# Optimization experiments

Measured on AMD Instinct MI355X. Metric: run time of the kernel, lower is better.

The kernel has to match this reference:

```python
import jax, jax.numpy as jnp
import numpy as np

B, T, C = 2, 2048, 1024
N_HEAD = 16
HEAD_DIM = C // N_HEAD


def setup_inputs() -> dict:
    key = jax.random.key(0)
    k1, k2, k3 = jax.random.split(key, 3)
    s = 1.0 / np.sqrt(C)
    return {
        "x": jax.random.normal(k1, (B, T, C), dtype=jnp.float32),
        "w_qkv": jax.random.normal(k2, (C, 3 * C), dtype=jnp.float32) * s,
        "b_qkv": jnp.zeros((3 * C,), dtype=jnp.float32),
        "w_out": jax.random.normal(k3, (C, C), dtype=jnp.float32) * s,
        "b_out": jnp.zeros((C,), dtype=jnp.float32),
    }


def reference(x, w_qkv, b_qkv, w_out, b_out):
    b, t, c = x.shape
    qkv = x @ w_qkv + b_qkv                                   # [B,T,3C]
    # Faithful to torch: view(B,T,H,3*hd).transpose(1,2) then split last dim
    qkv = qkv.reshape(b, t, N_HEAD, 3 * HEAD_DIM).transpose(0, 2, 1, 3)  # [B,H,T,3hd]
    q, k, v = jnp.split(qkv, 3, axis=-1)                      # each [B,H,T,hd]
    att = jnp.einsum("bhqd,bhkd->bhqk", q, k) / np.sqrt(HEAD_DIM)
    causal = jnp.tril(jnp.ones((t, t), dtype=bool))
    att = jnp.where(causal[None, None], att, -jnp.inf)
    att = jax.nn.softmax(att, axis=-1)                        # dropout p=0 (eval)
    y = jnp.einsum("bhqk,bhkd->bhqd", att, v)                 # [B,H,T,hd]
    y = y.transpose(0, 2, 1, 3).reshape(b, t, c)
    return y @ w_out + b_out
```

## Files before the change

### kernel.cpp

```cpp
#include <hip/hip_runtime.h>


#define T_SEQ 2048
#define C_DIM 1024
#define NH    16
#define HD    64
#define BT    4096

typedef short bf16x8 __attribute__((ext_vector_type(8)));
typedef float floatx4 __attribute__((ext_vector_type(4)));

static __device__ __forceinline__ unsigned short f2bf(float f) {
    union { float f; unsigned u; } v; v.f = f;
    unsigned u = v.u;
    return (unsigned short)((u + 0x7FFFu + ((u >> 16) & 1u)) >> 16);
}
static __device__ __forceinline__ float bf2f(unsigned short u) {
    union { unsigned u; float f; } v; v.u = ((unsigned)u) << 16; return v.f;
}
static __device__ __forceinline__ float exp2_fast(float x) {
    float r; asm("v_exp_f32 %0, %1" : "=v"(r) : "v"(x)); return r;
}
static __device__ __forceinline__ unsigned cvt_pk_bf16(float lo, float hi) {
    unsigned r; asm("v_cvt_pk_bf16_f32 %0, %1, %2" : "=v"(r) : "v"(lo), "v"(hi)); return r;
}

static __device__ __forceinline__ void gl2lds16(const void* g, void* l) {
    __builtin_amdgcn_global_load_lds(
        (const __attribute__((address_space(1))) unsigned int*)g,
        (__attribute__((address_space(3))) unsigned int*)l, 16, 0, 0);
}

static __device__ __forceinline__ void transpose_body(float (*tile)[65],
                                                      const float* __restrict__ W,
                                                      unsigned short* __restrict__ Wt,
                                                      int K, int N, int bx, int by) {
    const int k0 = by << 6;
    const int n0 = bx << 6;
    const int rr = threadIdx.x >> 4;
    const int cc = (threadIdx.x & 15) << 2;
#pragma unroll
    for (int i = 0; i < 4; i++) {
        int r = rr + (i << 4);
        *(float4*)&tile[r][cc] = *(const float4*)(W + (size_t)(k0 + r) * N + n0 + cc);
    }
    __syncthreads();
#pragma unroll
    for (int i = 0; i < 4; i++) {
        int nr = rr + (i << 4);
        ushort4 o;
        o.x = f2bf(tile[cc + 0][nr]);
        o.y = f2bf(tile[cc + 1][nr]);
        o.z = f2bf(tile[cc + 2][nr]);
        o.w = f2bf(tile[cc + 3][nr]);
        *(ushort4*)(Wt + (size_t)(n0 + nr) * K + k0 + cc) = o;
    }
}

__global__ __launch_bounds__(256) void prep(const float* __restrict__ x,
                                            unsigned short* __restrict__ xb,
                                            const float* __restrict__ w_qkv,
                                            unsigned short* __restrict__ wqkvT,
                                            const float* __restrict__ w_out,
                                            unsigned short* __restrict__ woutT) {
    __shared__ float tile[64][65];
    const int bx = blockIdx.x;
    if (bx < 1024) {
        int i = (bx * 256 + threadIdx.x) * 4;
        const int n = BT * C_DIM;
        const int stride = 1024 * 1024;
        for (; i < n; i += stride) {
            float4 f = *(const float4*)(x + i);
            ushort4 o;
            o.x = f2bf(f.x); o.y = f2bf(f.y); o.z = f2bf(f.z); o.w = f2bf(f.w);
            *(ushort4*)(xb + i) = o;
        }
    } else if (bx < 1024 + 768) {
        int b = bx - 1024;
        transpose_body(tile, w_qkv, wqkvT, 1024, 3072, b % 48, b / 48);
    } else {
        int b = bx - 1024 - 768;
        transpose_body(tile, w_out, woutT, 1024, 1024, b % 16, b / 16);
    }
}

#define GEMM_CORE(A_, Bt_, K_)                                                      \
    __shared__ short As[128 * 64];                                                  \
    __shared__ short Bs[128 * 64];                                                  \
    const int tid  = threadIdx.x;                                                   \
    const int lane = tid & 63, wave = tid >> 6;                                     \
    const int ln   = lane & 15, quad = lane >> 4;                                   \
    const int wm   = wave & 1,  wn   = wave >> 1;                                   \
    const int row0 = blockIdx.y << 7;                                               \
    const int col0 = blockIdx.x << 7;                                               \
    floatx4 acc[4][4];                                                              \
    _Pragma("unroll")                                                               \
    for (int i = 0; i < 4; i++)                                                     \
        _Pragma("unroll")                                                           \
        for (int j = 0; j < 4; j++) acc[i][j] = (floatx4){0.f, 0.f, 0.f, 0.f};      \
    for (int k0 = 0; k0 < K_; k0 += 64) {                                           \
        _Pragma("unroll")                                                           \
        for (int i = 0; i < 4; i++) {                                               \
            int c = (i << 8) + tid;                                                 \
            int r = c >> 3;                                                         \
            int gsrc = (c & 7) ^ (r & 7);                                           \
            gl2lds16(A_  + (size_t)(row0 + r) * K_ + k0 + (gsrc << 3), &As[c << 3]); \
            gl2lds16(Bt_ + (size_t)(col0 + r) * K_ + k0 + (gsrc << 3), &Bs[c << 3]); \
        }                                                                           \
        __syncthreads();                                                            \
        _Pragma("unroll")                                                           \
        for (int half = 0; half < 2; half++) {                                      \
            bf16x8 af[4], bfr[4];                                                   \
            _Pragma("unroll")                                                       \
            for (int t4 = 0; t4 < 4; t4++) {                                        \
                int ra = (wm << 6) + (t4 << 4) + ln;                                \
                int rb = (wn << 6) + (t4 << 4) + ln;                                \
                int g  = (half << 2) + quad;                                        \
                af[t4]  = *(bf16x8*)&As[((ra << 3) + (g ^ (ra & 7))) << 3];         \
                bfr[t4] = *(bf16x8*)&Bs[((rb << 3) + (g ^ (rb & 7))) << 3];         \
            }                                                                       \
            _Pragma("unroll")                                                       \
            for (int mt = 0; mt < 4; mt++)                                          \
                _Pragma("unroll")                                                   \
                for (int nt = 0; nt < 4; nt++)                                      \
                    acc[mt][nt] = __builtin_amdgcn_mfma_f32_16x16x32_bf16(af[mt], bfr[nt], acc[mt][nt], 0, 0, 0); \
        }                                                                           \
        __syncthreads();                                                            \
    }

__global__ __launch_bounds__(256) void gemm_qkv(const unsigned short* __restrict__ A,
                                                const unsigned short* __restrict__ Bt,
                                                const float* __restrict__ bias,
                                                unsigned short* __restrict__ qb,
                                                unsigned short* __restrict__ kb,
                                                unsigned short* __restrict__ vt) {
    GEMM_CORE(A, Bt, 1024)
    const float QSCALE = 0.125f * 1.4426950408889634f;
#pragma unroll
    for (int mt = 0; mt < 4; mt++) {
#pragma unroll
        for (int nt = 0; nt < 4; nt++) {
            int n = col0 + (wn << 6) + (nt << 4) + ln;
            int h = n / 192, r = n % 192;
            int sel = r >> 6, d = r & 63;
            float bv = bias[n];
            int m0 = row0 + (wm << 6) + (mt << 4) + (quad << 2);
            int b  = m0 >> 11, t0 = m0 & 2047;
            if (sel == 2) {
                ushort4 o4;
                o4.x = f2bf(acc[mt][nt][0] + bv);
                o4.y = f2bf(acc[mt][nt][1] + bv);
                o4.z = f2bf(acc[mt][nt][2] + bv);
                o4.w = f2bf(acc[mt][nt][3] + bv);
                *(ushort4*)(vt + (((size_t)(b * NH + h)) * HD + d) * T_SEQ + t0) = o4;
            } else if (sel == 0) {
#pragma unroll
                for (int e = 0; e < 4; e++) {
                    size_t idx = (((size_t)(b * NH + h)) * T_SEQ + t0 + e) * HD + d;
                    qb[idx] = f2bf((acc[mt][nt][e] + bv) * QSCALE);
                }
            } else {
#pragma unroll
                for (int e = 0; e < 4; e++) {
                    size_t idx = (((size_t)(b * NH + h)) * T_SEQ + t0 + e) * HD + d;
                    kb[idx] = f2bf(acc[mt][nt][e] + bv);
                }
            }
        }
    }
}

__global__ __launch_bounds__(256) void gemm_out(const unsigned short* __restrict__ A,
                                                const unsigned short* __restrict__ Bt,
                                                const float* __restrict__ bias,
                                                float* __restrict__ out) {
    const int K = 1024, N = 1024;
    __shared__ short As[128 * 64];
    __shared__ short Bs[64 * 64];
    const int tid  = threadIdx.x;
    const int lane = tid & 63, wave = tid >> 6;
    const int ln   = lane & 15, quad = lane >> 4;
    const int wm   = wave & 1,  wn   = wave >> 1;
    const int row0 = blockIdx.y << 7;
    const int col0 = blockIdx.x << 6;
    floatx4 acc[4][2];
#pragma unroll
    for (int i = 0; i < 4; i++)
#pragma unroll
        for (int j = 0; j < 2; j++) acc[i][j] = (floatx4){0.f, 0.f, 0.f, 0.f};
    for (int k0 = 0; k0 < K; k0 += 64) {
#pragma unroll
        for (int i = 0; i < 4; i++) {
            int c = (i << 8) + tid;
            int r = c >> 3;
            int gsrc = (c & 7) ^ (r & 7);
            gl2lds16(A + (size_t)(row0 + r) * K + k0 + (gsrc << 3), &As[c << 3]);
        }
#pragma unroll
        for (int i = 0; i < 2; i++) {
            int c = (i << 8) + tid;
            int r = c >> 3;
            int gsrc = (c & 7) ^ (r & 7);
            gl2lds16(Bt + (size_t)(col0 + r) * K + k0 + (gsrc << 3), &Bs[c << 3]);
        }
        __syncthreads();
#pragma unroll
        for (int half = 0; half < 2; half++) {
            bf16x8 af[4], bfr[2];
#pragma unroll
            for (int t4 = 0; t4 < 4; t4++) {
                int ra = (wm << 6) + (t4 << 4) + ln;
                int g  = (half << 2) + quad;
                af[t4] = *(bf16x8*)&As[((ra << 3) + (g ^ (ra & 7))) << 3];
            }
#pragma unroll
            for (int t2 = 0; t2 < 2; t2++) {
                int rb = (wn << 5) + (t2 << 4) + ln;
                int g  = (half << 2) + quad;
                bfr[t2] = *(bf16x8*)&Bs[((rb << 3) + (g ^ (rb & 7))) << 3];
            }
#pragma unroll
            for (int mt = 0; mt < 4; mt++)
#pragma unroll
                for (int nt = 0; nt < 2; nt++)
                    acc[mt][nt] = __builtin_amdgcn_mfma_f32_16x16x32_bf16(af[mt], bfr[nt], acc[mt][nt], 0, 0, 0);
        }
        __syncthreads();
    }
#pragma unroll
    for (int mt = 0; mt < 4; mt++) {
#pragma unroll
        for (int nt = 0; nt < 2; nt++) {
            int n = col0 + (wn << 5) + (nt << 4) + ln;
            float bv = bias[n];
#pragma unroll
            for (int e = 0; e < 4; e++) {
                int m = row0 + (wm << 6) + (mt << 4) + (quad << 2) + e;
                out[(size_t)m * N + n] = acc[mt][nt][e] + bv;
            }
        }
    }
}

__global__ __launch_bounds__(256, 4) void attn_p1(const unsigned short* __restrict__ qb,
                                                  const unsigned short* __restrict__ kb,
                                                  const unsigned short* __restrict__ vt,
                                                  unsigned short* __restrict__ y,
                                                  unsigned short* __restrict__ po,
                                                  float* __restrict__ pm,
                                                  float* __restrict__ pl) {
    __shared__ short Ks[64][68];
    __shared__ short Vs[64][68];
    __shared__ short QP[64][68];
    const int tid  = threadIdx.x;
    const int w    = tid >> 6, lane = tid & 63;
    const int ln   = lane & 15, quad = lane >> 4;

    const int L     = blockIdx.y * 80 + blockIdx.x;
    const int xcd   = L & 7;
    const int slotL = L >> 3;
    const int bh    = xcd + ((slotL / 80) << 3);
    const int bx    = slotL % 80;

    int qt, c;
    if (bx < 32)      { qt = 31 - bx;        c = 0; }
    else if (bx < 56) { qt = 31 - (bx - 32); c = 1; }
    else if (bx < 72) { qt = 31 - (bx - 56); c = 2; }
    else              { qt = 31 - (bx - 72); c = 3; }
    const int kt_lo = c << 3;
    const int kt_hi = (kt_lo + 7 < qt) ? (kt_lo + 7) : qt;
    const int nc    = (qt >> 3) + 1;
    const bool fin  = (nc == 1);
    const size_t base = (size_t)bh * T_SEQ * HD;
    const int q0   = qt << 6;
    const int sb   = q0 + (w << 4);
    const float NEG_INF = -__builtin_inff();

    const int sr = tid >> 3;
    const int sc = (tid & 7) << 3;

    const unsigned short* qrow = qb + base + (size_t)(q0 + (w << 4) + ln) * HD;
    bf16x8 bq0 = *(const bf16x8*)(qrow + (quad << 3));
    bf16x8 bq1 = *(const bf16x8*)(qrow + 32 + (quad << 3));

    bf16x8 kreg[2], vreg[2];
    const int kk0 = kt_lo << 6;
#pragma unroll
    for (int i = 0; i < 2; i++) {
        kreg[i] = *(const bf16x8*)(kb + base + (size_t)(kk0 + sr + (i << 5)) * HD + sc);
        vreg[i] = *(const bf16x8*)(vt + base + (size_t)(sr + (i << 5)) * T_SEQ + kk0 + sc);
    }

    floatx4 o[4];
#pragma unroll
    for (int nt = 0; nt < 4; nt++) o[nt] = (floatx4){0.f, 0.f, 0.f, 0.f};
    float m_prev = NEG_INF, l_run = 0.f;

    for (int kt = kt_lo; kt <= kt_hi; kt++) {
        const int k0 = kt << 6;
        __syncthreads();
#pragma unroll
        for (int i = 0; i < 2; i++) {
            *(bf16x8*)&Ks[sr + (i << 5)][sc] = kreg[i];
            *(bf16x8*)&Vs[sr + (i << 5)][sc] = vreg[i];
        }
        __syncthreads();
        if (kt < kt_hi) {
            const int kn = k0 + 64;
#pragma unroll
            for (int i = 0; i < 2; i++) {
                kreg[i] = *(const bf16x8*)(kb + base + (size_t)(kn + sr + (i << 5)) * HD + sc);
                vreg[i] = *(const bf16x8*)(vt + base + (size_t)(sr + (i << 5)) * T_SEQ + kn + sc);
            }
        }

        const bool diag  = (kt == qt);
        const int  nlive = diag ? w : 3;

        floatx4 st[4];
        __builtin_amdgcn_s_setprio(1);
#pragma unroll
        for (int ktl = 0; ktl < 4; ktl++) {
            if (ktl <= nlive) {
                bf16x8 a0 = *(bf16x8*)&Ks[(ktl << 4) + ln][quad << 3];
                bf16x8 a1 = *(bf16x8*)&Ks[(ktl << 4) + ln][32 + (quad << 3)];
                floatx4 acc = (floatx4){0.f, 0.f, 0.f, 0.f};
                acc = __builtin_amdgcn_mfma_f32_16x16x32_bf16(a0, bq0, acc, 0, 0, 0);
                acc = __builtin_amdgcn_mfma_f32_16x16x32_bf16(a1, bq1, acc, 0, 0, 0);
                st[ktl] = acc;
            }
        }
        __builtin_amdgcn_s_setprio(0);
        if (diag) {
#pragma unroll
            for (int ktl = 0; ktl < 4; ktl++) {
                if (ktl <= nlive) {
#pragma unroll
                    for (int e = 0; e < 4; e++) {
                        int kg = k0 + (ktl << 4) + (quad << 2) + e;
                        if (kg > sb + ln) st[ktl][e] = NEG_INF;
                    }
                }
            }
        }

        float mx = NEG_INF;
#pragma unroll
        for (int ktl = 0; ktl < 4; ktl++)
            if (ktl <= nlive) {
                mx = fmaxf(mx, fmaxf(fmaxf(st[ktl][0], st[ktl][1]),
                                     fmaxf(st[ktl][2], st[ktl][3])));
            }
        mx = fmaxf(mx, __shfl_xor(mx, 16));
        mx = fmaxf(mx, __shfl_xor(mx, 32));
        const bool need = __any(mx > m_prev);
        const float m_new = fmaxf(m_prev, mx);
        float psum = 0.f;
#pragma unroll
        for (int ktl = 0; ktl < 4; ktl++)
            if (ktl <= nlive) {
#pragma unroll
                for (int e = 0; e < 4; e++) {
                    float p = exp2_fast(st[ktl][e] - m_new);
                    st[ktl][e] = p;
                    psum += p;
                }
            }
        psum += __shfl_xor(psum, 16);
        psum += __shfl_xor(psum, 32);

#pragma unroll
        for (int ktl = 0; ktl < 4; ktl++) {
            uint2 pw;
            if (ktl <= nlive) {
                pw.x = cvt_pk_bf16(st[ktl][0], st[ktl][1]);
                pw.y = cvt_pk_bf16(st[ktl][2], st[ktl][3]);
            } else {
                pw.x = 0; pw.y = 0;
            }
            *(uint2*)&QP[(w << 4) + ln][(ktl << 4) + (quad << 2)] = pw;
        }

        if (need) {
            float alpha = exp2_fast(m_prev - m_new);
            float arow[4];
#pragma unroll
            for (int e = 0; e < 4; e++) arow[e] = __shfl(alpha, (quad << 2) + e);
#pragma unroll
            for (int nt = 0; nt < 4; nt++)
#pragma unroll
                for (int e = 0; e < 4; e++) o[nt][e] *= arow[e];
            l_run = l_run * alpha + psum;
            m_prev = m_new;
        } else {
            l_run += psum;
        }

        bf16x8 ap0 = *(bf16x8*)&QP[(w << 4) + ln][quad << 3];
        bf16x8 ap1 = *(bf16x8*)&QP[(w << 4) + ln][32 + (quad << 3)];
        __builtin_amdgcn_s_setprio(1);
#pragma unroll
        for (int nt = 0; nt < 4; nt++) {
            bf16x8 v0 = *(bf16x8*)&Vs[(nt << 4) + ln][quad << 3];
            bf16x8 v1 = *(bf16x8*)&Vs[(nt << 4) + ln][32 + (quad << 3)];
            o[nt] = __builtin_amdgcn_mfma_f32_16x16x32_bf16(ap0, v0, o[nt], 0, 0, 0);
            o[nt] = __builtin_amdgcn_mfma_f32_16x16x32_bf16(ap1, v1, o[nt], 0, 0, 0);
        }
        __builtin_amdgcn_s_setprio(0);
    }

    if (fin) {
        float linv[4];
#pragma unroll
        for (int e = 0; e < 4; e++) linv[e] = 1.0f / __shfl(l_run, (quad << 2) + e);
        const int b = bh >> 4, h = bh & 15;
#pragma unroll
        for (int e = 0; e < 4; e++) {
            int t = sb + (quad << 2) + e;
            unsigned short* yrow = y + ((size_t)b * T_SEQ + t) * C_DIM + h * HD;
#pragma unroll
            for (int nt = 0; nt < 4; nt++)
                yrow[(nt << 4) + ln] = f2bf(o[nt][e] * linv[e]);
        }
    } else {
        int cb;
        if (qt < 16)      cb = (qt - 8) * 2;
        else if (qt < 24) cb = 16 + (qt - 16) * 3;
        else              cb = 40 + (qt - 24) * 4;
        const int slot = bh * 72 + cb + c;
        if (quad == 0) {
            pm[(slot << 6) + (w << 4) + ln] = m_prev;
            pl[(slot << 6) + (w << 4) + ln] = l_run;
        }
#pragma unroll
        for (int e = 0; e < 4; e++) {
            int q = (w << 4) + (quad << 2) + e;
            unsigned short* porow = po + (((size_t)slot << 6) + q) * HD;
#pragma unroll
            for (int nt = 0; nt < 4; nt++)
                porow[(nt << 4) + ln] = f2bf(o[nt][e]);
        }
    }
}

__global__ __launch_bounds__(256) void attn_p2(const unsigned short* __restrict__ po,
                                               const float* __restrict__ pm,
                                               const float* __restrict__ pl,
                                               unsigned short* __restrict__ y) {
    const int qt = 8 + blockIdx.x;
    const int bh = blockIdx.y;
    const int nc = (qt >> 3) + 1;
    int cb;
    if (qt < 16)      cb = (qt - 8) * 2;
    else if (qt < 24) cb = 16 + (qt - 16) * 3;
    else              cb = 40 + (qt - 24) * 4;
    const int slot0 = bh * 72 + cb;
    const int tid = threadIdx.x;
    const int q  = tid >> 2;
    const int d0 = (tid & 3) << 4;
    const float NEG_INF = -__builtin_inff();

    float mv[4], lv[4];
#pragma unroll
    for (int cc = 0; cc < 4; cc++) {
        if (cc < nc) {
            mv[cc] = pm[((slot0 + cc) << 6) + q];
            lv[cc] = pl[((slot0 + cc) << 6) + q];
        } else {
            mv[cc] = NEG_INF; lv[cc] = 0.f;
        }
    }
    float m = fmaxf(fmaxf(mv[0], mv[1]), fmaxf(mv[2], mv[3]));
    float a[4];
    float L = 0.f;
#pragma unroll
    for (int cc = 0; cc < 4; cc++) {
        a[cc] = (cc < nc) ? exp2_fast(mv[cc] - m) : 0.f;
        L += lv[cc] * a[cc];
    }
    const float inv = 1.0f / L;
#pragma unroll
    for (int cc = 0; cc < 4; cc++) a[cc] *= inv;

    float acc[16];
#pragma unroll
    for (int i = 0; i < 16; i++) acc[i] = 0.f;
#pragma unroll
    for (int cc = 0; cc < 4; cc++) {
        if (cc < nc) {
            const unsigned short* r = po + (((size_t)(slot0 + cc)) << 12) + (q << 6) + d0;
            const float ac = a[cc];
#pragma unroll
            for (int i = 0; i < 4; i++) {
                ushort4 u = *(const ushort4*)(r + (i << 2));
                acc[(i << 2) + 0] += ac * bf2f(u.x);
                acc[(i << 2) + 1] += ac * bf2f(u.y);
                acc[(i << 2) + 2] += ac * bf2f(u.z);
                acc[(i << 2) + 3] += ac * bf2f(u.w);
            }
        }
    }

    const int b = bh >> 4, h = bh & 15;
    const int t = (qt << 6) + q;
    unsigned short* yrow = y + ((size_t)b * T_SEQ + t) * C_DIM + h * HD + d0;
#pragma unroll
    for (int i = 0; i < 4; i++) {
        ushort4 ow;
        ow.x = f2bf(acc[(i << 2) + 0]);
        ow.y = f2bf(acc[(i << 2) + 1]);
        ow.z = f2bf(acc[(i << 2) + 2]);
        ow.w = f2bf(acc[(i << 2) + 3]);
        *(ushort4*)(yrow + (i << 2)) = ow;
    }
}

extern "C" void kernel_launch(void* const* d_in, const int* in_sizes, int n_in,
                              void* d_out, int out_size, void* d_ws, size_t ws_size,
                              hipStream_t stream) {
    (void)in_sizes; (void)n_in; (void)out_size; (void)ws_size;
    const float* x     = (const float*)d_in[0];
    const float* w_qkv = (const float*)d_in[1];
    const float* b_qkv = (const float*)d_in[2];
    const float* w_out = (const float*)d_in[3];
    const float* b_out = (const float*)d_in[4];
    float* out = (float*)d_out;

    char* ws = (char*)d_ws;
    unsigned short* qb    = (unsigned short*)ws;
    unsigned short* kb    = (unsigned short*)(ws + ((size_t)8  << 20));
    unsigned short* vt    = (unsigned short*)(ws + ((size_t)16 << 20));
    unsigned short* xb    = (unsigned short*)(ws + ((size_t)24 << 20));
    unsigned short* yb    = xb;
    unsigned short* woutT = (unsigned short*)(ws + ((size_t)32 << 20));
    unsigned short* wqkvT = (unsigned short*)(ws + ((size_t)42 << 20));
    unsigned short* po    = (unsigned short*)(ws + ((size_t)34 << 20));
    float*          pm    = (float*)(ws + ((size_t)52 << 20));
    float*          pl    = (float*)(ws + ((size_t)52 << 20) + (640 << 10));

    prep    <<<2048, 256, 0, stream>>>(x, xb, w_qkv, wqkvT, w_out, woutT);
    gemm_qkv<<<dim3(24, 32), 256, 0, stream>>>(xb, wqkvT, b_qkv, qb, kb, vt);
    attn_p1 <<<dim3(80, 32), 256, 0, stream>>>(qb, kb, vt, yb, po, pm, pl);
    attn_p2 <<<dim3(24, 32), 256, 0, stream>>>(po, pm, pl, yb);
    gemm_out<<<dim3(16, 32), 256, 0, stream>>>(yb, woutT, b_out, out);
}
```

Before: 197.2 us.

## Swizzle GEMM blocks per XCD, transpose QKV epilogue, hoist V loads, defer l reductions

```diff
diff --git a/kernel.cpp b/kernel.cpp
--- a/kernel.cpp
+++ b/kernel.cpp
@@ -84,87 +84,89 @@
     }
 }
 
-#define GEMM_CORE(A_, Bt_, K_)                                                      \
-    __shared__ short As[128 * 64];                                                  \
-    __shared__ short Bs[128 * 64];                                                  \
-    const int tid  = threadIdx.x;                                                   \
-    const int lane = tid & 63, wave = tid >> 6;                                     \
-    const int ln   = lane & 15, quad = lane >> 4;                                   \
-    const int wm   = wave & 1,  wn   = wave >> 1;                                   \
-    const int row0 = blockIdx.y << 7;                                               \
-    const int col0 = blockIdx.x << 7;                                               \
-    floatx4 acc[4][4];                                                              \
-    _Pragma("unroll")                                                               \
-    for (int i = 0; i < 4; i++)                                                     \
-        _Pragma("unroll")                                                           \
-        for (int j = 0; j < 4; j++) acc[i][j] = (floatx4){0.f, 0.f, 0.f, 0.f};      \
-    for (int k0 = 0; k0 < K_; k0 += 64) {                                           \
-        _Pragma("unroll")                                                           \
-        for (int i = 0; i < 4; i++) {                                               \
-            int c = (i << 8) + tid;                                                 \
-            int r = c >> 3;                                                         \
-            int gsrc = (c & 7) ^ (r & 7);                                           \
-            gl2lds16(A_  + (size_t)(row0 + r) * K_ + k0 + (gsrc << 3), &As[c << 3]); \
-            gl2lds16(Bt_ + (size_t)(col0 + r) * K_ + k0 + (gsrc << 3), &Bs[c << 3]); \
-        }                                                                           \
-        __syncthreads();                                                            \
-        _Pragma("unroll")                                                           \
-        for (int half = 0; half < 2; half++) {                                      \
-            bf16x8 af[4], bfr[4];                                                   \
-            _Pragma("unroll")                                                       \
-            for (int t4 = 0; t4 < 4; t4++) {                                        \
-                int ra = (wm << 6) + (t4 << 4) + ln;                                \
-                int rb = (wn << 6) + (t4 << 4) + ln;                                \
-                int g  = (half << 2) + quad;                                        \
-                af[t4]  = *(bf16x8*)&As[((ra << 3) + (g ^ (ra & 7))) << 3];         \
-                bfr[t4] = *(bf16x8*)&Bs[((rb << 3) + (g ^ (rb & 7))) << 3];         \
-            }                                                                       \
-            _Pragma("unroll")                                                       \
-            for (int mt = 0; mt < 4; mt++)                                          \
-                _Pragma("unroll")                                                   \
-                for (int nt = 0; nt < 4; nt++)                                      \
-                    acc[mt][nt] = __builtin_amdgcn_mfma_f32_16x16x32_bf16(af[mt], bfr[nt], acc[mt][nt], 0, 0, 0); \
-        }                                                                           \
-        __syncthreads();                                                            \
-    }
-
 __global__ __launch_bounds__(256) void gemm_qkv(const unsigned short* __restrict__ A,
                                                 const unsigned short* __restrict__ Bt,
                                                 const float* __restrict__ bias,
                                                 unsigned short* __restrict__ qb,
                                                 unsigned short* __restrict__ kb,
                                                 unsigned short* __restrict__ vt) {
-    GEMM_CORE(A, Bt, 1024)
+    __shared__ short As[128 * 64];
+    __shared__ short Bs[128 * 64];
+    const int K_ = 1024;
+    const int tid  = threadIdx.x;
+    const int lane = tid & 63, wave = tid >> 6;
+    const int ln   = lane & 15, quad = lane >> 4;
+    const int wm   = wave & 1,  wn   = wave >> 1;
+    const int L    = blockIdx.y * 24 + blockIdx.x;
+    const int xcd  = L & 7, idx = L >> 3;
+    const int row0 = ((xcd << 2) + idx / 24) << 7;
+    const int col0 = (idx % 24) << 7;
+    floatx4 acc[4][4];
+#pragma unroll
+    for (int i = 0; i < 4; i++)
+#pragma unroll
+        for (int j = 0; j < 4; j++) acc[i][j] = (floatx4){0.f, 0.f, 0.f, 0.f};
+    for (int k0 = 0; k0 < K_; k0 += 64) {
+#pragma unroll
+        for (int i = 0; i < 4; i++) {
+            int c = (i << 8) + tid;
+            int r = c >> 3;
+            int gsrc = (c & 7) ^ (r & 7);
+            gl2lds16(A  + (size_t)(row0 + r) * K_ + k0 + (gsrc << 3), &As[c << 3]);
+            gl2lds16(Bt + (size_t)(col0 + r) * K_ + k0 + (gsrc << 3), &Bs[c << 3]);
+        }
+        __syncthreads();
+#pragma unroll
+        for (int half = 0; half < 2; half++) {
+            bf16x8 af[4], bfr[4];
+#pragma unroll
+            for (int t4 = 0; t4 < 4; t4++) {
+                int ra = (wm << 6) + (t4 << 4) + ln;
+                int rb = (wn << 6) + (t4 << 4) + ln;
+                int g  = (half << 2) + quad;
+                af[t4]  = *(bf16x8*)&As[((ra << 3) + (g ^ (ra & 7))) << 3];
+                bfr[t4] = *(bf16x8*)&Bs[((rb << 3) + (g ^ (rb & 7))) << 3];
+            }
+#pragma unroll
+            for (int mt = 0; mt < 4; mt++)
+#pragma unroll
+                for (int nt = 0; nt < 4; nt++)
+                    acc[mt][nt] = __builtin_amdgcn_mfma_f32_16x16x32_bf16(bfr[nt], af[mt], acc[mt][nt], 0, 0, 0);
+        }
+        __syncthreads();
+    }
     const float QSCALE = 0.125f * 1.4426950408889634f;
 #pragma unroll
-    for (int mt = 0; mt < 4; mt++) {
-#pragma unroll
-        for (int nt = 0; nt < 4; nt++) {
-            int n = col0 + (wn << 6) + (nt << 4) + ln;
-            int h = n / 192, r = n % 192;
-            int sel = r >> 6, d = r & 63;
-            float bv = bias[n];
-            int m0 = row0 + (wm << 6) + (mt << 4) + (quad << 2);
-            int b  = m0 >> 11, t0 = m0 & 2047;
-            if (sel == 2) {
+    for (int nt = 0; nt < 4; nt++) {
+        const int n0  = col0 + (wn << 6) + (nt << 4) + (quad << 2);
+        const int h   = n0 / 192;
+        const int r   = n0 % 192;
+        const int sel = r >> 6, d0 = r & 63;
+        const float4 bv4 = *(const float4*)(bias + n0);
+        const float bv[4] = {bv4.x, bv4.y, bv4.z, bv4.w};
+#pragma unroll
+        for (int mt = 0; mt < 4; mt++) {
+            const int m = row0 + (wm << 6) + (mt << 4) + ln;
+            const int b = m >> 11, t = m & 2047;
+            const size_t bhh = (size_t)(b * NH + h);
+            if (sel == 0) {
                 ushort4 o4;
-                o4.x = f2bf(acc[mt][nt][0] + bv);
-                o4.y = f2bf(acc[mt][nt][1] + bv);
-                o4.z = f2bf(acc[mt][nt][2] + bv);
-                o4.w = f2bf(acc[mt][nt][3] + bv);
-                *(ushort4*)(vt + (((size_t)(b * NH + h)) * HD + d) * T_SEQ + t0) = o4;
-            } else if (sel == 0) {
-#pragma unroll
-                for (int e = 0; e < 4; e++) {
-                    size_t idx = (((size_t)(b * NH + h)) * T_SEQ + t0 + e) * HD + d;
-                    qb[idx] = f2bf((acc[mt][nt][e] + bv) * QSCALE);
-                }
+                o4.x = f2bf((acc[mt][nt][0] + bv[0]) * QSCALE);
+                o4.y = f2bf((acc[mt][nt][1] + bv[1]) * QSCALE);
+                o4.z = f2bf((acc[mt][nt][2] + bv[2]) * QSCALE);
+                o4.w = f2bf((acc[mt][nt][3] + bv[3]) * QSCALE);
+                *(ushort4*)(qb + (bhh * T_SEQ + t) * HD + d0) = o4;
+            } else if (sel == 1) {
+                ushort4 o4;
+                o4.x = f2bf(acc[mt][nt][0] + bv[0]);
+                o4.y = f2bf(acc[mt][nt][1] + bv[1]);
+                o4.z = f2bf(acc[mt][nt][2] + bv[2]);
+                o4.w = f2bf(acc[mt][nt][3] + bv[3]);
+                *(ushort4*)(kb + (bhh * T_SEQ + t) * HD + d0) = o4;
             } else {
 #pragma unroll
-                for (int e = 0; e < 4; e++) {
-                    size_t idx = (((size_t)(b * NH + h)) * T_SEQ + t0 + e) * HD + d;
-                    kb[idx] = f2bf(acc[mt][nt][e] + bv);
-                }
+                for (int e = 0; e < 4; e++)
+                    vt[(bhh * HD + d0 + e) * T_SEQ + t] = f2bf(acc[mt][nt][e] + bv[e]);
             }
         }
     }
@@ -181,8 +183,10 @@
     const int lane = tid & 63, wave = tid >> 6;
     const int ln   = lane & 15, quad = lane >> 4;
     const int wm   = wave & 1,  wn   = wave >> 1;
-    const int row0 = blockIdx.y << 7;
-    const int col0 = blockIdx.x << 6;
+    const int L    = blockIdx.y * 16 + blockIdx.x;
+    const int xcd  = L & 7, idx = L >> 3;
+    const int row0 = ((xcd << 2) + (idx >> 4)) << 7;
+    const int col0 = (idx & 15) << 6;
     floatx4 acc[4][2];
 #pragma unroll
     for (int i = 0; i < 4; i++)
@@ -314,6 +318,13 @@
             }
         }
 
+        bf16x8 vf0[4], vf1[4];
+#pragma unroll
+        for (int nt = 0; nt < 4; nt++) {
+            vf0[nt] = *(bf16x8*)&Vs[(nt << 4) + ln][quad << 3];
+            vf1[nt] = *(bf16x8*)&Vs[(nt << 4) + ln][32 + (quad << 3)];
+        }
+
         const bool diag  = (kt == qt);
         const int  nlive = diag ? w : 3;
 
@@ -366,8 +377,6 @@
                     psum += p;
                 }
             }
-        psum += __shfl_xor(psum, 16);
-        psum += __shfl_xor(psum, 32);
 
 #pragma unroll
         for (int ktl = 0; ktl < 4; ktl++) {
@@ -401,13 +410,14 @@
         __builtin_amdgcn_s_setprio(1);
 #pragma unroll
         for (int nt = 0; nt < 4; nt++) {
-            bf16x8 v0 = *(bf16x8*)&Vs[(nt << 4) + ln][quad << 3];
-            bf16x8 v1 = *(bf16x8*)&Vs[(nt << 4) + ln][32 + (quad << 3)];
-            o[nt] = __builtin_amdgcn_mfma_f32_16x16x32_bf16(ap0, v0, o[nt], 0, 0, 0);
-            o[nt] = __builtin_amdgcn_mfma_f32_16x16x32_bf16(ap1, v1, o[nt], 0, 0, 0);
+            o[nt] = __builtin_amdgcn_mfma_f32_16x16x32_bf16(ap0, vf0[nt], o[nt], 0, 0, 0);
+            o[nt] = __builtin_amdgcn_mfma_f32_16x16x32_bf16(ap1, vf1[nt], o[nt], 0, 0, 0);
         }
         __builtin_amdgcn_s_setprio(0);
     }
+
+    l_run += __shfl_xor(l_run, 16);
+    l_run += __shfl_xor(l_run, 32);
 
     if (fin) {
         float linv[4];
```

Measured after the change: 199.5 us. About the same (+1.2%).
